# Kernel optimization log

Measured on AMD Instinct MI355X. Metric: run time of the kernel, lower is better.

## Reference

```python
import jax, jax.numpy as jnp
import numpy as np
from jax import lax

DN = ('NCDHW', 'OIDHW', 'NCDHW')

def _reflect_conv(s, w, pad_dhw):
    # s: [B,2,D,H,W]; reflect-pad spatial dims then VALID conv -> same spatial size
    p = jnp.pad(s, ((0, 0), (0, 0)) + pad_dhw, mode='reflect')
    return lax.conv_general_dilated(p, w, window_strides=(1, 1, 1),
                                    padding='VALID', dimension_numbers=DN)

def setup_inputs() -> dict:
    key = jax.random.key(0)
    k = jax.random.split(key, 5)
    x = jax.random.normal(k[0], (4, 32, 16, 128, 128), dtype=jnp.float32)
    w1 = jax.random.normal(k[1], (1, 2, 7, 7, 5), dtype=jnp.float32) * 0.1
    w2 = jax.random.normal(k[2], (1, 2, 5, 5, 3), dtype=jnp.float32) * 0.1
    w3 = jax.random.normal(k[3], (1, 2, 3, 3, 1), dtype=jnp.float32) * 0.2
    wf = jax.random.normal(k[4], (1, 3, 1, 1, 1), dtype=jnp.float32) * 0.5
    return {'x': x, 'w1': w1, 'w2': w2, 'w3': w3, 'wf': wf}

def reference(x, w1, w2, w3, wf):
    # channel pool: mean & max over channel dim -> [B,2,D,H,W]
    s_in = jnp.concatenate([jnp.mean(x, axis=1, keepdims=True),
                            jnp.max(x, axis=1, keepdims=True)], axis=1)
    # branch pads in (D,H,W) order match kernels (7,7,5)/(5,5,3)/(3,3,1)
    s1 = _reflect_conv(s_in, w1, ((3, 3), (3, 3), (2, 2)))
    s2 = _reflect_conv(s_in, w2, ((2, 2), (2, 2), (1, 1)))
    s3 = _reflect_conv(s_in, w3, ((1, 1), (1, 1), (0, 0)))
    s = jnp.concatenate([s1, s2, s3], axis=1)  # [B,3,D,H,W]
    fused = lax.conv_general_dilated(s, wf, window_strides=(1, 1, 1),
                                     padding='VALID', dimension_numbers=DN)
    spatial_weight = jax.nn.sigmoid(fused)  # [B,1,D,H,W]
    return x * spatial_weight
```

## Files before the change

### kernel.cpp

```cpp
#include <hip/hip_runtime.h>
#include <math.h>

#define B_ 4
#define C_ 32
#define D_ 16
#define H_ 128
#define W_ 128
#define HW_ (H_*W_)
#define SP_ (D_*HW_)

#define PW_ 136
#define PPL_ (H_*PW_)
#define PCH_ (D_*PPL_)

typedef float f32x4 __attribute__((ext_vector_type(4)));
typedef float f32x4u __attribute__((ext_vector_type(4), aligned(4)));

__device__ __forceinline__ int refl(int i, int n) {
    i = (i < 0) ? -i : i;
    i = (i >= n) ? (2*n - 2 - i) : i;
    return i;
}

__global__ void prep_weights_kernel(const float* __restrict__ w1,
                                    const float* __restrict__ w2,
                                    const float* __restrict__ w3,
                                    const float* __restrict__ wf,
                                    float* __restrict__ Wc) {
    int t = blockIdx.x * blockDim.x + threadIdx.x;
    if (t >= 2*7*7*5) return;
    int ow = t % 5;
    int oh = (t / 5) % 7;
    int od = (t / 35) % 7;
    int ci = t / 245;
    float v = wf[0] * w1[((ci*7+od)*7+oh)*5+ow];
    if (od>=1 && od<=5 && oh>=1 && oh<=5 && ow>=1 && ow<=3)
        v = fmaf(wf[1], w2[((ci*5+(od-1))*5+(oh-1))*3+(ow-1)], v);
    if (od>=2 && od<=4 && oh>=2 && oh<=4 && ow==2)
        v = fmaf(wf[2], w3[(ci*3+(od-2))*3+(oh-2)], v);
    Wc[t] = v;
}

__global__ __launch_bounds__(256) void pool_kernel(const float* __restrict__ x,
                                                   float* __restrict__ s) {
    int t = blockIdx.x * blockDim.x + threadIdx.x;
    if (t >= B_*D_*H_*(W_/4)) return;
    int w4 = (t % (W_/4)) * 4;
    int rest = t / (W_/4);
    int h = rest % H_;
    int bd = rest / H_;
    int d = bd % D_;
    int b = bd / D_;
    const float* xp = x + (b*C_*D_ + d)*HW_ + h*W_ + w4;
    f32x4 v = *(const f32x4*)xp;
    f32x4 sm = v, mx = v;
    #pragma unroll 8
    for (int c = 1; c < C_; ++c) {
        f32x4 u = *(const f32x4*)(xp + c*SP_);
        sm += u;
        mx.x=fmaxf(mx.x,u.x); mx.y=fmaxf(mx.y,u.y); mx.z=fmaxf(mx.z,u.z); mx.w=fmaxf(mx.w,u.w);
    }
    sm *= (1.0f/32.0f);
    float* rm = s + (b*2+0)*PCH_ + d*PPL_ + h*PW_;
    float* rM = s + (b*2+1)*PCH_ + d*PPL_ + h*PW_;
    *(f32x4u*)(rm + w4 + 2) = sm;
    *(f32x4u*)(rM + w4 + 2) = mx;
    if (w4 == 0) {
        rm[0] = sm.z; rm[1] = sm.y;
        rM[0] = mx.z; rM[1] = mx.y;
    } else if (w4 == 124) {
        rm[130] = sm.z; rm[131] = sm.y;
        rM[130] = mx.z; rM[131] = mx.y;
    }
}

__global__ __launch_bounds__(256, 2) void spatial_att_kernel(
        const float* __restrict__ x,
        const float* __restrict__ s,
        const float* __restrict__ Wc,
        float* __restrict__ out) {
    int bid = blockIdx.x;
    int ht = bid & 15;
    int dp = (bid >> 4) & 7;
    int b  = bid >> 7;
    int t = threadIdx.x;
    int w0 = (t & 31) * 4;
    int h0 = ht * 8 + (t >> 5);
    int d0 = dp * 2;

    int drow[8];
    #pragma unroll
    for (int k = 0; k < 8; ++k) drow[k] = refl(d0 + k - 3, D_) * PPL_;

    float acc0[4] = {0.f, 0.f, 0.f, 0.f};
    float acc1[4] = {0.f, 0.f, 0.f, 0.f};

    for (int ci = 0; ci < 2; ++ci) {
        const float* sc = s + (b*2 + ci)*PCH_;
        const float* wcb_ci = Wc + ci*245;
        for (int oh = 0; oh < 7; ++oh) {
            const float* sh = sc + refl(h0 + oh - 3, H_)*PW_ + w0;
            const float* wcb = wcb_ci + oh*5;
            #pragma unroll
            for (int k = 0; k < 8; ++k) {
                const float* rp = sh + drow[k];
                const f32x4 L = *(const f32x4*)(rp);
                const f32x4 R = *(const f32x4*)(rp + 4);
                float v[8] = {L.x, L.y, L.z, L.w, R.x, R.y, R.z, R.w};
                if (k <= 6) {
                    const float* wp = wcb + k*35;
                    #pragma unroll
                    for (int ow = 0; ow < 5; ++ow) {
                        float wgt = wp[ow];
                        #pragma unroll
                        for (int wi = 0; wi < 4; ++wi)
                            acc0[wi] = fmaf(wgt, v[wi+ow], acc0[wi]);
                    }
                }
                if (k >= 1) {
                    const float* wp = wcb + (k-1)*35;
                    #pragma unroll
                    for (int ow = 0; ow < 5; ++ow) {
                        float wgt = wp[ow];
                        #pragma unroll
                        for (int wi = 0; wi < 4; ++wi)
                            acc1[wi] = fmaf(wgt, v[wi+ow], acc1[wi]);
                    }
                }
            }
        }
    }

    float sg0[4], sg1[4];
    #pragma unroll
    for (int wi = 0; wi < 4; ++wi) {
        sg0[wi] = 1.0f/(1.0f + __expf(-acc0[wi]));
        sg1[wi] = 1.0f/(1.0f + __expf(-acc1[wi]));
    }

    int obase = (b*C_*D_ + d0)*HW_ + h0*W_ + w0;
    #pragma unroll 8
    for (int c = 0; c < C_; ++c) {
        int i0 = obase + c*SP_;
        f32x4 xv0 = *(const f32x4*)(x + i0);
        f32x4 xv1 = *(const f32x4*)(x + i0 + HW_);
        f32x4 o0; o0.x=xv0.x*sg0[0]; o0.y=xv0.y*sg0[1]; o0.z=xv0.z*sg0[2]; o0.w=xv0.w*sg0[3];
        f32x4 o1; o1.x=xv1.x*sg1[0]; o1.y=xv1.y*sg1[1]; o1.z=xv1.z*sg1[2]; o1.w=xv1.w*sg1[3];
        *(f32x4*)(out + i0) = o0;
        *(f32x4*)(out + i0 + HW_) = o1;
    }
}

extern "C" void kernel_launch(void* const* d_in, const int* in_sizes, int n_in,
                              void* d_out, int out_size, void* d_ws, size_t ws_size,
                              hipStream_t stream) {
    const float* x  = (const float*)d_in[0];
    const float* w1 = (const float*)d_in[1];
    const float* w2 = (const float*)d_in[2];
    const float* w3 = (const float*)d_in[3];
    const float* wf = (const float*)d_in[4];
    float* out = (float*)d_out;
    float* Wc = (float*)d_ws;
    float* s  = (float*)d_ws + 512;

    prep_weights_kernel<<<1, 512, 0, stream>>>(w1, w2, w3, wf, Wc);
    pool_kernel<<<(B_*D_*H_*(W_/4) + 255)/256, 256, 0, stream>>>(x, s);
    spatial_att_kernel<<<B_*(D_/2)*(H_/8), 256, 0, stream>>>(x, s, Wc, out);
}
```

Before: 84.75 us.

## Fuse weight prep, pooling and attention into one cooperative kernel with grid sync

Merges the three kernels into a single cooperative launch of 512 blocks. Each block first pools its share of channels, then waits at a grid-wide barrier and computes its attention tile. This removes two kernel launches and the gaps between them. In exchange it adds grid-sync overhead, caps the grid at the number of co-resident blocks, and keeps the old three-kernel path as a fallback if the cooperative launch fails.

```diff
diff --git a/kernel.cpp b/kernel.cpp
--- a/kernel.cpp
+++ b/kernel.cpp
@@ -1,5 +1,8 @@
 #include <hip/hip_runtime.h>
+#include <hip/hip_cooperative_groups.h>
 #include <math.h>
+
+namespace cg = cooperative_groups;
 
 #define B_ 4
 #define C_ 32
@@ -22,13 +25,11 @@
     return i;
 }
 
-__global__ void prep_weights_kernel(const float* __restrict__ w1,
-                                    const float* __restrict__ w2,
-                                    const float* __restrict__ w3,
-                                    const float* __restrict__ wf,
-                                    float* __restrict__ Wc) {
-    int t = blockIdx.x * blockDim.x + threadIdx.x;
-    if (t >= 2*7*7*5) return;
+__device__ __forceinline__ void prep_one(int t, const float* __restrict__ w1,
+                                         const float* __restrict__ w2,
+                                         const float* __restrict__ w3,
+                                         const float* __restrict__ wf,
+                                         float* __restrict__ Wc) {
     int ow = t % 5;
     int oh = (t / 5) % 7;
     int od = (t / 35) % 7;
@@ -41,49 +42,47 @@
     Wc[t] = v;
 }
 
-__global__ __launch_bounds__(256) void pool_kernel(const float* __restrict__ x,
-                                                   float* __restrict__ s) {
-    int t = blockIdx.x * blockDim.x + threadIdx.x;
-    if (t >= B_*D_*H_*(W_/4)) return;
-    int w4 = (t % (W_/4)) * 4;
-    int rest = t / (W_/4);
-    int h = rest % H_;
-    int bd = rest / H_;
-    int d = bd % D_;
-    int b = bd / D_;
-    const float* xp = x + (b*C_*D_ + d)*HW_ + h*W_ + w4;
-    f32x4 v = *(const f32x4*)xp;
-    f32x4 sm = v, mx = v;
-    #pragma unroll 8
-    for (int c = 1; c < C_; ++c) {
-        f32x4 u = *(const f32x4*)(xp + c*SP_);
-        sm += u;
-        mx.x=fmaxf(mx.x,u.x); mx.y=fmaxf(mx.y,u.y); mx.z=fmaxf(mx.z,u.z); mx.w=fmaxf(mx.w,u.w);
-    }
-    sm *= (1.0f/32.0f);
-    float* rm = s + (b*2+0)*PCH_ + d*PPL_ + h*PW_;
-    float* rM = s + (b*2+1)*PCH_ + d*PPL_ + h*PW_;
-    *(f32x4u*)(rm + w4 + 2) = sm;
-    *(f32x4u*)(rM + w4 + 2) = mx;
-    if (w4 == 0) {
-        rm[0] = sm.z; rm[1] = sm.y;
-        rM[0] = mx.z; rM[1] = mx.y;
-    } else if (w4 == 124) {
-        rm[130] = sm.z; rm[131] = sm.y;
-        rM[130] = mx.z; rM[131] = mx.y;
-    }
-}
-
-__global__ __launch_bounds__(256, 2) void spatial_att_kernel(
-        const float* __restrict__ x,
-        const float* __restrict__ s,
-        const float* __restrict__ Wc,
-        float* __restrict__ out) {
-    int bid = blockIdx.x;
-    int ht = bid & 15;
-    int dp = (bid >> 4) & 7;
-    int b  = bid >> 7;
-    int t = threadIdx.x;
+__device__ __forceinline__ void pool_share(int bid, int t,
+        const float* __restrict__ x, float* __restrict__ s) {
+    int p = bid >> 3;
+    int pb = p >> 4, pd = p & 15;
+    int h0b = (bid & 7) * 16;
+    #pragma unroll
+    for (int rep = 0; rep < 2; ++rep) {
+        int it = t + rep*256;
+        int w4 = (it & 31) * 4;
+        int h  = h0b + (it >> 5);
+        const float* xp = x + (pb*C_*D_ + pd)*HW_ + h*W_ + w4;
+        f32x4 v = *(const f32x4*)xp;
+        f32x4 sm = v, mx = v;
+        #pragma unroll 8
+        for (int c = 1; c < C_; ++c) {
+            f32x4 u = *(const f32x4*)(xp + c*SP_);
+            sm += u;
+            mx.x=fmaxf(mx.x,u.x); mx.y=fmaxf(mx.y,u.y);
+            mx.z=fmaxf(mx.z,u.z); mx.w=fmaxf(mx.w,u.w);
+        }
+        sm *= (1.0f/32.0f);
+        float* rm = s + (pb*2+0)*PCH_ + pd*PPL_ + h*PW_;
+        float* rM = s + (pb*2+1)*PCH_ + pd*PPL_ + h*PW_;
+        *(f32x4u*)(rm + w4 + 2) = sm;
+        *(f32x4u*)(rM + w4 + 2) = mx;
+        if (w4 == 0) {
+            rm[0] = sm.z; rm[1] = sm.y;
+            rM[0] = mx.z; rM[1] = mx.y;
+        } else if (w4 == 124) {
+            rm[130] = sm.z; rm[131] = sm.y;
+            rM[130] = mx.z; rM[131] = mx.y;
+        }
+    }
+}
+
+__device__ __forceinline__ void att_tile(int abid, int t,
+        const float* __restrict__ x, const float* __restrict__ s,
+        const float* __restrict__ Wc, float* __restrict__ out) {
+    int ht = abid & 15;
+    int dp = (abid >> 4) & 7;
+    int b  = abid >> 7;
     int w0 = (t & 31) * 4;
     int h0 = ht * 8 + (t >> 5);
     int d0 = dp * 2;
@@ -151,6 +150,50 @@
     }
 }
 
+__global__ __launch_bounds__(256, 2) void fused_coop_kernel(
+        const float* __restrict__ x,
+        float* __restrict__ s,
+        float* __restrict__ Wc,
+        float* __restrict__ out,
+        const float* __restrict__ w1,
+        const float* __restrict__ w2,
+        const float* __restrict__ w3,
+        const float* __restrict__ wf) {
+    int bid = blockIdx.x;
+    int t = threadIdx.x;
+    if (bid == 0) {
+        if (t < 245) prep_one(t, w1, w2, w3, wf, Wc);
+        int t2 = t + 245;
+        if (t2 < 490) prep_one(t2, w1, w2, w3, wf, Wc);
+    }
+    pool_share(bid, t, x, s);
+    cg::this_grid().sync();
+    att_tile(bid, t, x, s, Wc, out);
+}
+
+__global__ void prep_weights_kernel(const float* __restrict__ w1,
+                                    const float* __restrict__ w2,
+                                    const float* __restrict__ w3,
+                                    const float* __restrict__ wf,
+                                    float* __restrict__ Wc) {
+    int t = blockIdx.x * blockDim.x + threadIdx.x;
+    if (t < 2*7*7*5) prep_one(t, w1, w2, w3, wf, Wc);
+}
+
+__global__ __launch_bounds__(256) void pool_kernel(const float* __restrict__ x,
+                                                   float* __restrict__ s) {
+    int bid = blockIdx.x;
+    if (bid < 512) pool_share(bid, threadIdx.x, x, s);
+}
+
+__global__ __launch_bounds__(256, 2) void spatial_att_kernel(
+        const float* __restrict__ x,
+        const float* __restrict__ s,
+        const float* __restrict__ Wc,
+        float* __restrict__ out) {
+    att_tile(blockIdx.x, threadIdx.x, x, s, Wc, out);
+}
+
 extern "C" void kernel_launch(void* const* d_in, const int* in_sizes, int n_in,
                               void* d_out, int out_size, void* d_ws, size_t ws_size,
                               hipStream_t stream) {
@@ -163,7 +206,14 @@
     float* Wc = (float*)d_ws;
     float* s  = (float*)d_ws + 512;
 
-    prep_weights_kernel<<<1, 512, 0, stream>>>(w1, w2, w3, wf, Wc);
-    pool_kernel<<<(B_*D_*H_*(W_/4) + 255)/256, 256, 0, stream>>>(x, s);
-    spatial_att_kernel<<<B_*(D_/2)*(H_/8), 256, 0, stream>>>(x, s, Wc, out);
-}
+    void* args[] = {(void*)&x, (void*)&s, (void*)&Wc, (void*)&out,
+                    (void*)&w1, (void*)&w2, (void*)&w3, (void*)&wf};
+    hipError_t err = hipLaunchCooperativeKernel((void*)fused_coop_kernel,
+                                                dim3(512), dim3(256),
+                                                args, 0, stream);
+    if (err != hipSuccess) {
+        prep_weights_kernel<<<1, 512, 0, stream>>>(w1, w2, w3, wf, Wc);
+        pool_kernel<<<512, 256, 0, stream>>>(x, s);
+        spatial_att_kernel<<<B_*(D_/2)*(H_/8), 256, 0, stream>>>(x, s, Wc, out);
+    }
+}
```

Result: slower. 156.4 us (+84.6%).

## Split pool and attention passes by batch half and fold weight prep into pool

Applied to the files above, without the earlier changes.

The batch is split into two halves, each run as a pool launch followed by an attention launch, so the attention pass re-reads x from a smaller working set that is more likely to still be in cache. The separate weight-combining kernel is removed: one extra block in the first pool launch does that work. The trade-off is one more launch overall and half as many blocks per attention launch, which may leave compute units underused.

```diff
diff --git a/kernel.cpp b/kernel.cpp
--- a/kernel.cpp
+++ b/kernel.cpp
@@ -22,13 +22,11 @@
     return i;
 }
 
-__global__ void prep_weights_kernel(const float* __restrict__ w1,
-                                    const float* __restrict__ w2,
-                                    const float* __restrict__ w3,
-                                    const float* __restrict__ wf,
-                                    float* __restrict__ Wc) {
-    int t = blockIdx.x * blockDim.x + threadIdx.x;
-    if (t >= 2*7*7*5) return;
+__device__ __forceinline__ void prep_one(int t, const float* __restrict__ w1,
+                                         const float* __restrict__ w2,
+                                         const float* __restrict__ w3,
+                                         const float* __restrict__ wf,
+                                         float* __restrict__ Wc) {
     int ow = t % 5;
     int oh = (t / 5) % 7;
     int od = (t / 35) % 7;
@@ -41,16 +39,25 @@
     Wc[t] = v;
 }
 
-__global__ __launch_bounds__(256) void pool_kernel(const float* __restrict__ x,
-                                                   float* __restrict__ s) {
-    int t = blockIdx.x * blockDim.x + threadIdx.x;
-    if (t >= B_*D_*H_*(W_/4)) return;
-    int w4 = (t % (W_/4)) * 4;
-    int rest = t / (W_/4);
-    int h = rest % H_;
-    int bd = rest / H_;
-    int d = bd % D_;
-    int b = bd / D_;
+__global__ __launch_bounds__(256) void pool_kernel(
+        const float* __restrict__ x, float* __restrict__ s,
+        const float* __restrict__ w1, const float* __restrict__ w2,
+        const float* __restrict__ w3, const float* __restrict__ wf,
+        float* __restrict__ Wc, int b0) {
+    if (blockIdx.x >= 512) {
+        int t = threadIdx.x;
+        if (t < 245) prep_one(t, w1, w2, w3, wf, Wc);
+        int t2 = t + 245;
+        if (t2 < 490) prep_one(t2, w1, w2, w3, wf, Wc);
+        return;
+    }
+    int idx = blockIdx.x * 256 + threadIdx.x;
+    int w4 = (idx & 31) * 4;
+    int rest = idx >> 5;
+    int h = rest & 127;
+    int bd = rest >> 7;
+    int d = bd & 15;
+    int b = b0 + (bd >> 4);
     const float* xp = x + (b*C_*D_ + d)*HW_ + h*W_ + w4;
     f32x4 v = *(const f32x4*)xp;
     f32x4 sm = v, mx = v;
@@ -58,7 +65,8 @@
     for (int c = 1; c < C_; ++c) {
         f32x4 u = *(const f32x4*)(xp + c*SP_);
         sm += u;
-        mx.x=fmaxf(mx.x,u.x); mx.y=fmaxf(mx.y,u.y); mx.z=fmaxf(mx.z,u.z); mx.w=fmaxf(mx.w,u.w);
+        mx.x=fmaxf(mx.x,u.x); mx.y=fmaxf(mx.y,u.y);
+        mx.z=fmaxf(mx.z,u.z); mx.w=fmaxf(mx.w,u.w);
     }
     sm *= (1.0f/32.0f);
     float* rm = s + (b*2+0)*PCH_ + d*PPL_ + h*PW_;
@@ -78,11 +86,11 @@
         const float* __restrict__ x,
         const float* __restrict__ s,
         const float* __restrict__ Wc,
-        float* __restrict__ out) {
+        float* __restrict__ out, int b0) {
     int bid = blockIdx.x;
     int ht = bid & 15;
     int dp = (bid >> 4) & 7;
-    int b  = bid >> 7;
+    int b  = b0 + (bid >> 7);
     int t = threadIdx.x;
     int w0 = (t & 31) * 4;
     int h0 = ht * 8 + (t >> 5);
@@ -163,7 +171,8 @@
     float* Wc = (float*)d_ws;
     float* s  = (float*)d_ws + 512;
 
-    prep_weights_kernel<<<1, 512, 0, stream>>>(w1, w2, w3, wf, Wc);
-    pool_kernel<<<(B_*D_*H_*(W_/4) + 255)/256, 256, 0, stream>>>(x, s);
-    spatial_att_kernel<<<B_*(D_/2)*(H_/8), 256, 0, stream>>>(x, s, Wc, out);
+    pool_kernel<<<513, 256, 0, stream>>>(x, s, w1, w2, w3, wf, Wc, 0);
+    spatial_att_kernel<<<256, 256, 0, stream>>>(x, s, Wc, out, 0);
+    pool_kernel<<<512, 256, 0, stream>>>(x, s, w1, w2, w3, wf, Wc, 2);
+    spatial_att_kernel<<<256, 256, 0, stream>>>(x, s, Wc, out, 2);
 }
```

Measured after the change: 92.74 us. 9.4% more time.
